# Performance work log

Measured on AMD Instinct MI355X. Metric: run time of the kernel, lower is better.

Reference implementation:

```python
import jax, jax.numpy as jnp
import numpy as np

TOKENS = 16384
IN_F = 2048
OUT_F = 2048
RANK = 32
GROUP = 64          # int4 scale group size
PAD = 256           # token padding multiple used by the fused activation quantizer
QMAX = 7.0          # signed int4 symmetric quantization


def setup_inputs() -> dict:
    key = jax.random.key(0)
    ks = jax.random.split(key, 7)
    x = jax.random.normal(ks[0], (TOKENS, IN_F), dtype=jnp.float32)
    # packed int4 weights: two signed nibbles per int8 lane
    qweight = jax.random.randint(ks[1], (OUT_F, IN_F // 2), -128, 128, dtype=jnp.int8)
    # per-group weight scales [in//group, out], strictly positive
    wscales = jnp.abs(jax.random.normal(ks[2], (IN_F // GROUP, OUT_F), dtype=jnp.float32)) * 0.01 + 1e-4
    # activation smoothing factors, positive and near 1
    smooth_factor = jnp.abs(jax.random.normal(ks[3], (IN_F,), dtype=jnp.float32)) * 0.5 + 0.75
    bias = jax.random.normal(ks[4], (OUT_F,), dtype=jnp.float32) * 0.01
    proj_down = jax.random.normal(ks[5], (IN_F, RANK), dtype=jnp.float32) * 0.02
    proj_up = jax.random.normal(ks[6], (OUT_F, RANK), dtype=jnp.float32) * 0.02
    return {"x": x, "qweight": qweight, "wscales": wscales,
            "smooth_factor": smooth_factor, "bias": bias,
            "proj_down": proj_down, "proj_up": proj_up}


def _unpack_int4(qweight):
    # low nibble = even input channel, high nibble = odd input channel; arithmetic shifts keep sign
    low = jnp.right_shift(jnp.left_shift(qweight, 4), 4)
    high = jnpp = jnp.right_shift(qweight, 4)
    w = jnp.stack([low, high], axis=-1).reshape(qweight.shape[0], qweight.shape[1] * 2)
    return w.astype(jnp.float32)  # [out, in], values in [-8, 7]


def _forward(x, qweight, wscales, smooth_factor, bias, proj_down, proj_up):
    T = x.shape[0]
    t_pad = ((T + PAD - 1) // PAD) * PAD
    # activation smoothing
    xs = x / smooth_factor
    xs_p = jnp.pad(xs, ((0, t_pad - T), (0, 0)))
    # per-token per-64-group symmetric int4 activation quantization
    xg = xs_p.reshape(t_pad, IN_F // GROUP, GROUP)
    amax = jnp.max(jnp.abs(xg), axis=-1)                       # [Tp, G]
    ascales = jnp.where(amax > 0, amax / QMAX, jnp.float32(1.0))
    qx = jnp.clip(jnp.round(xg / ascales[..., None]), -8.0, 7.0)
    xdq = (qx * ascales[..., None]).reshape(t_pad, IN_F)       # dequantized activations
    # dequantize packed int4 weights with per-group scales
    w = _unpack_int4(qweight)                                  # [out, in]
    wdq = (w.reshape(OUT_F, IN_F // GROUP, GROUP) * wscales.T[:, :, None]).reshape(OUT_F, IN_F)
    # packed GEMM (dequantized equivalent) + fused low-rank residual + bias
    y = xdq @ wdq.T                                            # [Tp, out]
    y = y + (xs_p @ proj_down) @ proj_up.T + bias
    return y[:T]


def reference(x, qweight, wscales, smooth_factor, bias, proj_down, proj_up):
    return _forward(x, qweight, wscales, smooth_factor, bias, proj_down, proj_up)
```

## Files before the change

### kernel.cpp

```cpp
#include <hip/hip_runtime.h>

#define TOKENS 16384
#define THALF 8192
#define INF 2048
#define OUTF 2048
#define RANK 32
#define BM 128
#define BN 128
#define NKSTEP 64

typedef int   int32x4  __attribute__((ext_vector_type(4)));
typedef int   int32x2  __attribute__((ext_vector_type(2)));
typedef float floatx4  __attribute__((ext_vector_type(4)));
typedef short bf16x8   __attribute__((ext_vector_type(8)));
typedef _Float16 f16x8 __attribute__((ext_vector_type(8)));

typedef __attribute__((address_space(1))) const void gconst_t;
typedef __attribute__((address_space(3))) void ldsv_t;

__device__ __forceinline__ void gload_lds16(const void* g, void* l) {
  __builtin_amdgcn_global_load_lds((gconst_t*)g, (ldsv_t*)l, 16, 0, 0);
}

__device__ __forceinline__ unsigned short f2bf(float f) {
  unsigned u = __float_as_uint(f);
  unsigned r = (u + 0x7FFFu + ((u >> 16) & 1u)) >> 16;
  return (unsigned short)r;
}

__global__ __launch_bounds__(256) void unpack_kernel(const int* __restrict__ qw,
                                                     const float* __restrict__ wsc,
                                                     _Float16* __restrict__ wdq) {
  int idx = blockIdx.x * 256 + threadIdx.x;
  int o = idx >> 6;
  int ch = idx & 63;
  float ws = wsc[(size_t)(ch >> 1) * OUTF + o];
  const int4* src = (const int4*)qw + (size_t)idx * 4;
  _Float16* dst = wdq + (size_t)o * INF + ch * 32;
#pragma unroll
  for (int q = 0; q < 4; ++q) {
    int4 v = src[q];
    int e[4] = {v.x, v.y, v.z, v.w};
    alignas(16) _Float16 h[8];
#pragma unroll
    for (int j = 0; j < 4; ++j) {
      int lo = ((int)((unsigned)e[j] << 28)) >> 28;
      int hi = ((int)((unsigned)e[j] << 24)) >> 28;
      h[2 * j]     = (_Float16)((float)lo * ws);
      h[2 * j + 1] = (_Float16)((float)hi * ws);
    }
    *(int4*)(dst + q * 8) = *(const int4*)h;
  }
}

__global__ __launch_bounds__(256) void prep_pdT(const float* __restrict__ pd,
                                                unsigned short* __restrict__ pdT) {
  int idx = blockIdx.x * 256 + threadIdx.x;
  int r = idx >> 11, c = idx & 2047;
  pdT[idx] = f2bf(pd[(size_t)c * RANK + r]);
}

__global__ __launch_bounds__(256) void quant_kernel(
    const float* __restrict__ x, const float* __restrict__ smooth,
    const unsigned short* __restrict__ pdT,
    _Float16* __restrict__ xdq, float* __restrict__ tdown, int tbase) {
  __shared__ char lds[32768];
  int tid = threadIdx.x, lane = tid & 63, wid = tid >> 6;
  int t0rel = blockIdx.x * 32;
  int mi = wid >> 1, ni = wid & 1;
  floatx4 acc = {0.f, 0.f, 0.f, 0.f};

  floatx4 xv[8];
  floatx4 sm;
  int32x4 pv[4];

  auto issue_loads = [&](int kc) {
    const float* xb = x + (size_t)(tbase + t0rel + wid * 8) * INF + kc * 256 + lane * 4;
#pragma unroll
    for (int r = 0; r < 8; ++r) xv[r] = *(const floatx4*)(xb + r * INF);
    sm = *(const floatx4*)(smooth + kc * 256 + lane * 4);
#pragma unroll
    for (int q = 0; q < 4; ++q) {
      int flat = tid + q * 256;
      int row = flat >> 5, c16 = flat & 31;
      pv[q] = *(const int32x4*)((const char*)pdT + (size_t)row * 4096 + kc * 512 + c16 * 16);
    }
  };

  issue_loads(0);

  for (int kc = 0; kc < 8; ++kc) {
    floatx4 rsm;
    rsm[0] = 1.0f / sm[0]; rsm[1] = 1.0f / sm[1];
    rsm[2] = 1.0f / sm[2]; rsm[3] = 1.0f / sm[3];
#pragma unroll
    for (int q = 0; q < 4; ++q) {
      int flat = tid + q * 256;
      int row = flat >> 5, c16 = flat & 31;
      int byte = (row * 512 + c16 * 16) ^ ((row & 7) << 4);
      *(int32x4*)(lds + 16384 + byte) = pv[q];
    }
#pragma unroll
    for (int r = 0; r < 8; ++r) {
      floatx4 xs;
      xs[0] = xv[r][0] * rsm[0]; xs[1] = xv[r][1] * rsm[1];
      xs[2] = xv[r][2] * rsm[2]; xs[3] = xv[r][3] * rsm[3];
      float m4 = fmaxf(fmaxf(fabsf(xs[0]), fabsf(xs[1])),
                       fmaxf(fabsf(xs[2]), fabsf(xs[3])));
      m4 = fmaxf(m4, __shfl_xor(m4, 1, 64));
      m4 = fmaxf(m4, __shfl_xor(m4, 2, 64));
      m4 = fmaxf(m4, __shfl_xor(m4, 4, 64));
      m4 = fmaxf(m4, __shfl_xor(m4, 8, 64));
      float ascale = m4 > 0.f ? m4 / 7.0f : 1.0f;
      float rq = 1.0f / ascale;
      int tokrel = t0rel + wid * 8 + r;
      alignas(8) _Float16 hq[4];
#pragma unroll
      for (int b = 0; b < 4; ++b) {
        float qf = fminf(7.f, fmaxf(-8.f, rintf(xs[b] * rq)));
        hq[b] = (_Float16)(qf * ascale);
      }
      *(int32x2*)((char*)xdq + ((size_t)tokrel * INF + kc * 256 + lane * 4) * 2) =
          *(const int32x2*)hq;
      unsigned lo = (unsigned)f2bf(xs[0]) | ((unsigned)f2bf(xs[1]) << 16);
      unsigned hi = (unsigned)f2bf(xs[2]) | ((unsigned)f2bf(xs[3]) << 16);
      int lrow = wid * 8 + r;
      int xbyte = (lrow * 512 + lane * 8) ^ ((lrow & 7) << 4);
      int32x2 wv; wv[0] = (int)lo; wv[1] = (int)hi;
      *(int32x2*)(lds + xbyte) = wv;
    }
    __syncthreads();
    if (kc + 1 < 8) issue_loads(kc + 1);
#pragma unroll
    for (int ks = 0; ks < 8; ++ks) {
      int arow = mi * 16 + (lane & 15);
      int ab = (arow * 512 + ks * 64 + ((lane >> 4) << 4)) ^ ((arow & 7) << 4);
      bf16x8 av = *(const bf16x8*)(lds + ab);
      int brow = ni * 16 + (lane & 15);
      int bb = (brow * 512 + ks * 64 + ((lane >> 4) << 4)) ^ ((brow & 7) << 4);
      bf16x8 bv = *(const bf16x8*)(lds + 16384 + bb);
      acc = __builtin_amdgcn_mfma_f32_16x16x32_bf16(av, bv, acc, 0, 0, 0);
    }
    __syncthreads();
  }

  int trow = tbase + t0rel + mi * 16 + ((lane >> 4) << 2);
  int col = ni * 16 + (lane & 15);
#pragma unroll
  for (int r = 0; r < 4; ++r)
    tdown[(size_t)(trow + r) * RANK + col] = acc[r];
}

__global__ __launch_bounds__(256, 3) void gemm_kernel(
    const _Float16* __restrict__ xdq, const _Float16* __restrict__ wdq,
    const float* __restrict__ tdown, const float* __restrict__ pu,
    const float* __restrict__ bias, float* __restrict__ y,
    int tbase, int mPanels) {
  __shared__ char smem[49152];

  int tid = threadIdx.x;
  int lane = tid & 63;
  int wid = tid >> 6;
  int wr = wid >> 1, wc = wid & 1;

  int s = blockIdx.x;
  int xcd = s & 7, idx = s >> 3;
  int nloc = idx & 3, mloc = idx >> 2;
  int o0 = (((xcd & 3) << 2) + nloc) * BN;
  int t0rel = ((xcd >> 3 << 3) + (xcd >> 2) * (mPanels >> 1) + mloc) * BM;
  int t0abs = tbase + t0rel;

  floatx4 acc[4][4];
#pragma unroll
  for (int m = 0; m < 4; ++m)
#pragma unroll
    for (int n = 0; n < 4; ++n) acc[m][n] = (floatx4){0.f, 0.f, 0.f, 0.f};

  auto stage = [&](int g) {
    int bufb = (g % 3) * 16384;
#pragma unroll
    for (int i = 0; i < 2; ++i) {
      int c = tid + i * 256;
      int row = c >> 2;
      int l = (c & 3) ^ ((row >> 1) & 3);
      gload_lds16((const char*)xdq + (size_t)(t0rel + row) * (INF * 2) + g * 64 + l * 16,
                  smem + bufb + (wid + i * 4) * 1024);
      gload_lds16((const char*)wdq + (size_t)(o0 + row) * (INF * 2) + g * 64 + l * 16,
                  smem + bufb + 8192 + (wid + i * 4) * 1024);
    }
  };

  int aoff[4], boff[4];
#pragma unroll
  for (int m = 0; m < 4; ++m) {
    int arow = (wr << 6) + (m << 4) + (lane & 15);
    aoff[m] = arow * 64 + ((((lane >> 4)) ^ ((arow >> 1) & 3)) << 4);
    int brow = (wc << 6) + (m << 4) + (lane & 15);
    boff[m] = 8192 + brow * 64 + ((((lane >> 4)) ^ ((brow >> 1) & 3)) << 4);
  }

  stage(0);
  stage(1);

  for (int g = 0; g < NKSTEP; ++g) {
    if (g == NKSTEP - 1) asm volatile("s_waitcnt vmcnt(0)" ::: "memory");
    else                 asm volatile("s_waitcnt vmcnt(4)" ::: "memory");
    __builtin_amdgcn_s_barrier();
    __builtin_amdgcn_sched_barrier(0);

    if (g + 2 < NKSTEP) stage(g + 2);

    int bufb = (g % 3) * 16384;
    f16x8 af[4], bf_[4];
#pragma unroll
    for (int m = 0; m < 4; ++m) af[m] = *(const f16x8*)(smem + bufb + aoff[m]);
#pragma unroll
    for (int n = 0; n < 4; ++n) bf_[n] = *(const f16x8*)(smem + bufb + boff[n]);

#pragma unroll
    for (int m = 0; m < 4; ++m)
#pragma unroll
      for (int n = 0; n < 4; ++n)
        acc[m][n] = __builtin_amdgcn_mfma_f32_16x16x32_f16(af[m], bf_[n], acc[m][n], 0, 0, 0);
  }

  __syncthreads();

  unsigned short* td_lds = (unsigned short*)smem;
  unsigned short* pu_lds = (unsigned short*)(smem + 8192);
  {
    int row = tid >> 1, h = (tid & 1) * 16;
    const float* ts = tdown + (size_t)(t0abs + row) * RANK + h;
    const float* ps = pu + (size_t)(o0 + row) * RANK + h;
    unsigned tw[8], pw[8];
#pragma unroll
    for (int q = 0; q < 4; ++q) {
      float4 v = *(const float4*)(ts + q * 4);
      tw[q * 2 + 0] = (unsigned)f2bf(v.x) | ((unsigned)f2bf(v.y) << 16);
      tw[q * 2 + 1] = (unsigned)f2bf(v.z) | ((unsigned)f2bf(v.w) << 16);
      float4 p = *(const float4*)(ps + q * 4);
      pw[q * 2 + 0] = (unsigned)f2bf(p.x) | ((unsigned)f2bf(p.y) << 16);
      pw[q * 2 + 1] = (unsigned)f2bf(p.z) | ((unsigned)f2bf(p.w) << 16);
    }
    int4 s0, s1;
    s0.x = (int)tw[0]; s0.y = (int)tw[1]; s0.z = (int)tw[2]; s0.w = (int)tw[3];
    s1.x = (int)tw[4]; s1.y = (int)tw[5]; s1.z = (int)tw[6]; s1.w = (int)tw[7];
    *(int4*)(td_lds + row * 32 + h) = s0;
    *(int4*)(td_lds + row * 32 + h + 8) = s1;
    s0.x = (int)pw[0]; s0.y = (int)pw[1]; s0.z = (int)pw[2]; s0.w = (int)pw[3];
    s1.x = (int)pw[4]; s1.y = (int)pw[5]; s1.z = (int)pw[6]; s1.w = (int)pw[7];
    *(int4*)(pu_lds + row * 32 + h) = s0;
    *(int4*)(pu_lds + row * 32 + h + 8) = s1;
  }
  __syncthreads();

  bf16x8 ta[4], pb4[4];
  int koff8 = (lane >> 4) << 3;
#pragma unroll
  for (int m = 0; m < 4; ++m)
    ta[m] = *(const bf16x8*)&td_lds[((wr << 6) + (m << 4) + (lane & 15)) * 32 + koff8];
#pragma unroll
  for (int n = 0; n < 4; ++n)
    pb4[n] = *(const bf16x8*)&pu_lds[((wc << 6) + (n << 4) + (lane & 15)) * 32 + koff8];

#pragma unroll
  for (int n = 0; n < 4; ++n) {
    int oc = o0 + (wc << 6) + (n << 4) + (lane & 15);
    float bv = bias[oc];
#pragma unroll
    for (int m = 0; m < 4; ++m) {
      floatx4 c = acc[m][n];
      c = __builtin_amdgcn_mfma_f32_16x16x32_bf16(ta[m], pb4[n], c, 0, 0, 0);
#pragma unroll
      for (int r = 0; r < 4; ++r) {
        int tr = t0abs + (wr << 6) + (m << 4) + ((lane >> 4) << 2) + r;
        y[(size_t)tr * OUTF + oc] = c[r] + bv;
      }
    }
  }
}

extern "C" void kernel_launch(void* const* d_in, const int* in_sizes, int n_in,
                              void* d_out, int out_size, void* d_ws, size_t ws_size,
                              hipStream_t stream) {
  const float* x      = (const float*)d_in[0];
  const int*   qw     = (const int*)d_in[1];
  const float* wsc    = (const float*)d_in[2];
  const float* smooth = (const float*)d_in[3];
  const float* bias   = (const float*)d_in[4];
  const float* pd     = (const float*)d_in[5];
  const float* pu     = (const float*)d_in[6];
  float* y = (float*)d_out;

  char* ws = (char*)d_ws;
  unsigned short* pdT = (unsigned short*)((char*)d_out + (64u << 20));

  if (ws_size >= 77594624ULL) {
    _Float16* xdq = (_Float16*)ws;
    _Float16* wdq = (_Float16*)(ws + 67108864);
    float* tdown  = (float*)(ws + 67108864 + 8388608);
    unpack_kernel<<<512, 256, 0, stream>>>(qw, wsc, wdq);
    prep_pdT<<<256, 256, 0, stream>>>(pd, pdT);
    quant_kernel<<<TOKENS / 32, 256, 0, stream>>>(x, smooth, pdT, xdq, tdown, 0);
    gemm_kernel<<<16 * (TOKENS / BM), 256, 0, stream>>>(
        xdq, wdq, tdown, pu, bias, y, 0, TOKENS / BM);
  } else {
    _Float16* xdq = (_Float16*)ws;
    _Float16* wdq = (_Float16*)(ws + 33554432);
    float* tdown  = (float*)(ws + 33554432 + 8388608);
    unpack_kernel<<<512, 256, 0, stream>>>(qw, wsc, wdq);
    prep_pdT<<<256, 256, 0, stream>>>(pd, pdT);
    for (int c = 0; c < 2; ++c) {
      int tbase = c * THALF;
      quant_kernel<<<THALF / 32, 256, 0, stream>>>(x, smooth, pdT, xdq, tdown, tbase);
      gemm_kernel<<<16 * (THALF / BM), 256, 0, stream>>>(
          xdq, wdq, tdown, pu, bias, y, tbase, THALF / BM);
    }
  }
}
```

Before: 236.2 us.

## Enlarge GEMM tile to 256x128 with 8 waves and 64-deep K steps

The GEMM block tile grows from 128x128 to 256x128 with 512 threads (8 waves) per block, and each pipeline stage now loads a 64-element K slice instead of 32, halving the number of barrier-separated iterations. LDS use rises to 144 KB for the triple-buffered stages with a new 8-slot XOR swizzle. The aim is more reuse of each loaded weight tile, lower per-K-step sync overhead, and fewer blocks. In exchange occupancy per CU drops, the LDS footprint is large, and each block loads more per stage.

```diff
diff --git a/kernel.cpp b/kernel.cpp
--- a/kernel.cpp
+++ b/kernel.cpp
@@ -5,9 +5,9 @@
 #define INF 2048
 #define OUTF 2048
 #define RANK 32
-#define BM 128
+#define BM 256
 #define BN 128
-#define NKSTEP 64
+#define NPER 32
 
 typedef int   int32x4  __attribute__((ext_vector_type(4)));
 typedef int   int32x2  __attribute__((ext_vector_type(2)));
@@ -151,23 +151,24 @@
     tdown[(size_t)(trow + r) * RANK + col] = acc[r];
 }
 
-__global__ __launch_bounds__(256, 3) void gemm_kernel(
+__global__ __launch_bounds__(512, 2) void gemm_kernel(
     const _Float16* __restrict__ xdq, const _Float16* __restrict__ wdq,
     const float* __restrict__ tdown, const float* __restrict__ pu,
     const float* __restrict__ bias, float* __restrict__ y,
     int tbase, int mPanels) {
-  __shared__ char smem[49152];
+  __shared__ char smem[147456];
 
   int tid = threadIdx.x;
   int lane = tid & 63;
   int wid = tid >> 6;
-  int wr = wid >> 1, wc = wid & 1;
+  int wm = wid >> 1, wn = wid & 1;
 
   int s = blockIdx.x;
   int xcd = s & 7, idx = s >> 3;
-  int nloc = idx & 3, mloc = idx >> 2;
-  int o0 = (((xcd & 3) << 2) + nloc) * BN;
-  int t0rel = ((xcd >> 3 << 3) + (xcd >> 2) * (mPanels >> 1) + mloc) * BM;
+  int npan = ((xcd & 3) << 2) + (idx & 3);
+  int mpan = (xcd >> 2) * (mPanels >> 1) + (idx >> 2);
+  int o0 = npan * BN;
+  int t0rel = mpan * BM;
   int t0abs = tbase + t0rel;
 
   floatx4 acc[4][4];
@@ -177,80 +178,107 @@
     for (int n = 0; n < 4; ++n) acc[m][n] = (floatx4){0.f, 0.f, 0.f, 0.f};
 
   auto stage = [&](int g) {
-    int bufb = (g % 3) * 16384;
+    int bufb = (g % 3) * 49152;
+#pragma unroll
+    for (int i = 0; i < 4; ++i) {
+      int f = i * 512 + tid;
+      int row = f >> 3, sl = (f & 7) ^ (row & 7);
+      gload_lds16((const char*)xdq + (size_t)(t0rel + row) * (INF * 2) + g * 128 + sl * 16,
+                  smem + bufb + i * 8192 + wid * 1024);
+    }
 #pragma unroll
     for (int i = 0; i < 2; ++i) {
-      int c = tid + i * 256;
-      int row = c >> 2;
-      int l = (c & 3) ^ ((row >> 1) & 3);
-      gload_lds16((const char*)xdq + (size_t)(t0rel + row) * (INF * 2) + g * 64 + l * 16,
-                  smem + bufb + (wid + i * 4) * 1024);
-      gload_lds16((const char*)wdq + (size_t)(o0 + row) * (INF * 2) + g * 64 + l * 16,
-                  smem + bufb + 8192 + (wid + i * 4) * 1024);
+      int f = i * 512 + tid;
+      int row = f >> 3, sl = (f & 7) ^ (row & 7);
+      gload_lds16((const char*)wdq + (size_t)(o0 + row) * (INF * 2) + g * 128 + sl * 16,
+                  smem + bufb + 32768 + i * 8192 + wid * 1024);
     }
   };
 
-  int aoff[4], boff[4];
-#pragma unroll
-  for (int m = 0; m < 4; ++m) {
-    int arow = (wr << 6) + (m << 4) + (lane & 15);
-    aoff[m] = arow * 64 + ((((lane >> 4)) ^ ((arow >> 1) & 3)) << 4);
-    int brow = (wc << 6) + (m << 4) + (lane & 15);
-    boff[m] = 8192 + brow * 64 + ((((lane >> 4)) ^ ((brow >> 1) & 3)) << 4);
+  int aoff[4][2], boff[4][2];
+#pragma unroll
+  for (int mr = 0; mr < 4; ++mr) {
+    int r = (wm << 6) + (mr << 4) + (lane & 15);
+#pragma unroll
+    for (int ks = 0; ks < 2; ++ks) {
+      int sl = ((ks << 2) + (lane >> 4)) ^ (r & 7);
+      aoff[mr][ks] = r * 128 + sl * 16;
+    }
+  }
+#pragma unroll
+  for (int nr = 0; nr < 4; ++nr) {
+    int r = (wn << 6) + (nr << 4) + (lane & 15);
+#pragma unroll
+    for (int ks = 0; ks < 2; ++ks) {
+      int sl = ((ks << 2) + (lane >> 4)) ^ (r & 7);
+      boff[nr][ks] = 32768 + r * 128 + sl * 16;
+    }
   }
 
   stage(0);
   stage(1);
 
-  for (int g = 0; g < NKSTEP; ++g) {
-    if (g == NKSTEP - 1) asm volatile("s_waitcnt vmcnt(0)" ::: "memory");
-    else                 asm volatile("s_waitcnt vmcnt(4)" ::: "memory");
+  for (int g = 0; g < NPER; ++g) {
+    if (g == NPER - 1) asm volatile("s_waitcnt vmcnt(0)" ::: "memory");
+    else               asm volatile("s_waitcnt vmcnt(6)" ::: "memory");
     __builtin_amdgcn_s_barrier();
     __builtin_amdgcn_sched_barrier(0);
 
-    if (g + 2 < NKSTEP) stage(g + 2);
-
-    int bufb = (g % 3) * 16384;
-    f16x8 af[4], bf_[4];
-#pragma unroll
-    for (int m = 0; m < 4; ++m) af[m] = *(const f16x8*)(smem + bufb + aoff[m]);
-#pragma unroll
-    for (int n = 0; n < 4; ++n) bf_[n] = *(const f16x8*)(smem + bufb + boff[n]);
-
-#pragma unroll
-    for (int m = 0; m < 4; ++m)
-#pragma unroll
-      for (int n = 0; n < 4; ++n)
-        acc[m][n] = __builtin_amdgcn_mfma_f32_16x16x32_f16(af[m], bf_[n], acc[m][n], 0, 0, 0);
+    if (g + 2 < NPER) stage(g + 2);
+
+    int bufb = (g % 3) * 49152;
+    f16x8 af[2][4], bf_[2][4];
+#pragma unroll
+    for (int ks = 0; ks < 2; ++ks) {
+#pragma unroll
+      for (int mr = 0; mr < 4; ++mr) af[ks][mr] = *(const f16x8*)(smem + bufb + aoff[mr][ks]);
+#pragma unroll
+      for (int nr = 0; nr < 4; ++nr) bf_[ks][nr] = *(const f16x8*)(smem + bufb + boff[nr][ks]);
+    }
+
+#pragma unroll
+    for (int ks = 0; ks < 2; ++ks)
+#pragma unroll
+      for (int mr = 0; mr < 4; ++mr)
+#pragma unroll
+        for (int nr = 0; nr < 4; ++nr)
+          acc[mr][nr] = __builtin_amdgcn_mfma_f32_16x16x32_f16(af[ks][mr], bf_[ks][nr],
+                                                               acc[mr][nr], 0, 0, 0);
   }
 
   __syncthreads();
 
   unsigned short* td_lds = (unsigned short*)smem;
-  unsigned short* pu_lds = (unsigned short*)(smem + 8192);
+  unsigned short* pu_lds = (unsigned short*)(smem + 16384);
   {
     int row = tid >> 1, h = (tid & 1) * 16;
     const float* ts = tdown + (size_t)(t0abs + row) * RANK + h;
-    const float* ps = pu + (size_t)(o0 + row) * RANK + h;
-    unsigned tw[8], pw[8];
+    unsigned tw[8];
 #pragma unroll
     for (int q = 0; q < 4; ++q) {
       float4 v = *(const float4*)(ts + q * 4);
       tw[q * 2 + 0] = (unsigned)f2bf(v.x) | ((unsigned)f2bf(v.y) << 16);
       tw[q * 2 + 1] = (unsigned)f2bf(v.z) | ((unsigned)f2bf(v.w) << 16);
-      float4 p = *(const float4*)(ps + q * 4);
-      pw[q * 2 + 0] = (unsigned)f2bf(p.x) | ((unsigned)f2bf(p.y) << 16);
-      pw[q * 2 + 1] = (unsigned)f2bf(p.z) | ((unsigned)f2bf(p.w) << 16);
     }
     int4 s0, s1;
     s0.x = (int)tw[0]; s0.y = (int)tw[1]; s0.z = (int)tw[2]; s0.w = (int)tw[3];
     s1.x = (int)tw[4]; s1.y = (int)tw[5]; s1.z = (int)tw[6]; s1.w = (int)tw[7];
     *(int4*)(td_lds + row * 32 + h) = s0;
     *(int4*)(td_lds + row * 32 + h + 8) = s1;
-    s0.x = (int)pw[0]; s0.y = (int)pw[1]; s0.z = (int)pw[2]; s0.w = (int)pw[3];
-    s1.x = (int)pw[4]; s1.y = (int)pw[5]; s1.z = (int)pw[6]; s1.w = (int)pw[7];
-    *(int4*)(pu_lds + row * 32 + h) = s0;
-    *(int4*)(pu_lds + row * 32 + h + 8) = s1;
+    if (tid < 256) {
+      const float* ps = pu + (size_t)(o0 + row) * RANK + h;
+      unsigned pw[8];
+#pragma unroll
+      for (int q = 0; q < 4; ++q) {
+        float4 p = *(const float4*)(ps + q * 4);
+        pw[q * 2 + 0] = (unsigned)f2bf(p.x) | ((unsigned)f2bf(p.y) << 16);
+        pw[q * 2 + 1] = (unsigned)f2bf(p.z) | ((unsigned)f2bf(p.w) << 16);
+      }
+      s0.x = (int)pw[0]; s0.y = (int)pw[1]; s0.z = (int)pw[2]; s0.w = (int)pw[3];
+      s1.x = (int)pw[4]; s1.y = (int)pw[5]; s1.z = (int)pw[6]; s1.w = (int)pw[7];
+      *(int4*)(pu_lds + row * 32 + h) = s0;
+      *(int4*)(pu_lds + row * 32 + h + 8) = s1;
+    }
   }
   __syncthreads();
 
@@ -258,14 +286,14 @@
   int koff8 = (lane >> 4) << 3;
 #pragma unroll
   for (int m = 0; m < 4; ++m)
-    ta[m] = *(const bf16x8*)&td_lds[((wr << 6) + (m << 4) + (lane & 15)) * 32 + koff8];
+    ta[m] = *(const bf16x8*)&td_lds[((wm << 6) + (m << 4) + (lane & 15)) * 32 + koff8];
 #pragma unroll
   for (int n = 0; n < 4; ++n)
-    pb4[n] = *(const bf16x8*)&pu_lds[((wc << 6) + (n << 4) + (lane & 15)) * 32 + koff8];
+    pb4[n] = *(const bf16x8*)&pu_lds[((wn << 6) + (n << 4) + (lane & 15)) * 32 + koff8];
 
 #pragma unroll
   for (int n = 0; n < 4; ++n) {
-    int oc = o0 + (wc << 6) + (n << 4) + (lane & 15);
+    int oc = o0 + (wn << 6) + (n << 4) + (lane & 15);
     float bv = bias[oc];
 #pragma unroll
     for (int m = 0; m < 4; ++m) {
@@ -273,7 +301,7 @@
       c = __builtin_amdgcn_mfma_f32_16x16x32_bf16(ta[m], pb4[n], c, 0, 0, 0);
 #pragma unroll
       for (int r = 0; r < 4; ++r) {
-        int tr = t0abs + (wr << 6) + (m << 4) + ((lane >> 4) << 2) + r;
+        int tr = t0abs + (wm << 6) + (m << 4) + ((lane >> 4) << 2) + r;
         y[(size_t)tr * OUTF + oc] = c[r] + bv;
       }
     }
@@ -302,7 +330,7 @@
     unpack_kernel<<<512, 256, 0, stream>>>(qw, wsc, wdq);
     prep_pdT<<<256, 256, 0, stream>>>(pd, pdT);
     quant_kernel<<<TOKENS / 32, 256, 0, stream>>>(x, smooth, pdT, xdq, tdown, 0);
-    gemm_kernel<<<16 * (TOKENS / BM), 256, 0, stream>>>(
+    gemm_kernel<<<16 * (TOKENS / BM), 512, 0, stream>>>(
         xdq, wdq, tdown, pu, bias, y, 0, TOKENS / BM);
   } else {
     _Float16* xdq = (_Float16*)ws;
@@ -313,7 +341,7 @@
     for (int c = 0; c < 2; ++c) {
       int tbase = c * THALF;
       quant_kernel<<<THALF / 32, 256, 0, stream>>>(x, smooth, pdT, xdq, tdown, tbase);
-      gemm_kernel<<<16 * (THALF / BM), 256, 0, stream>>>(
+      gemm_kernel<<<16 * (THALF / BM), 512, 0, stream>>>(
           xdq, wdq, tdown, pu, bias, y, tbase, THALF / BM);
     }
   }
```

After: 220.8 us. 6.5% less time.

## Enlarge GEMM tile to 256x256 with 16-wave blocks and merge prep kernels

Applied to the files above, without the earlier changes.

The GEMM moves from 128x128 tiles with 4 waves to 256x256 tiles with 16 waves per 1024-thread block, each wave still computing a 64x64 sub-tile. LDS triple buffering doubles to 96 KB. The prefetch is now issued after the LDS fragment reads, and MFMA issue priority is raised with s_setprio. The aim is to halve global/L2 traffic per FLOP and cut the block count. The weight-unpack and projection-transpose kernels are merged into one launch. The cost is one block per CU with large LDS, so there is less latency hiding across blocks and a coarser tail.

```diff
diff --git a/kernel.cpp b/kernel.cpp
--- a/kernel.cpp
+++ b/kernel.cpp
@@ -5,9 +5,9 @@
 #define INF 2048
 #define OUTF 2048
 #define RANK 32
-#define BM 128
-#define BN 128
-#define NKSTEP 64
+#define BM 256
+#define BN 256
+#define NT 64
 
 typedef int   int32x4  __attribute__((ext_vector_type(4)));
 typedef int   int32x2  __attribute__((ext_vector_type(2)));
@@ -28,36 +28,38 @@
   return (unsigned short)r;
 }
 
-__global__ __launch_bounds__(256) void unpack_kernel(const int* __restrict__ qw,
-                                                     const float* __restrict__ wsc,
-                                                     _Float16* __restrict__ wdq) {
-  int idx = blockIdx.x * 256 + threadIdx.x;
-  int o = idx >> 6;
-  int ch = idx & 63;
-  float ws = wsc[(size_t)(ch >> 1) * OUTF + o];
-  const int4* src = (const int4*)qw + (size_t)idx * 4;
-  _Float16* dst = wdq + (size_t)o * INF + ch * 32;
-#pragma unroll
-  for (int q = 0; q < 4; ++q) {
-    int4 v = src[q];
-    int e[4] = {v.x, v.y, v.z, v.w};
-    alignas(16) _Float16 h[8];
-#pragma unroll
-    for (int j = 0; j < 4; ++j) {
-      int lo = ((int)((unsigned)e[j] << 28)) >> 28;
-      int hi = ((int)((unsigned)e[j] << 24)) >> 28;
-      h[2 * j]     = (_Float16)((float)lo * ws);
-      h[2 * j + 1] = (_Float16)((float)hi * ws);
-    }
-    *(int4*)(dst + q * 8) = *(const int4*)h;
-  }
-}
-
-__global__ __launch_bounds__(256) void prep_pdT(const float* __restrict__ pd,
-                                                unsigned short* __restrict__ pdT) {
-  int idx = blockIdx.x * 256 + threadIdx.x;
-  int r = idx >> 11, c = idx & 2047;
-  pdT[idx] = f2bf(pd[(size_t)c * RANK + r]);
+__global__ __launch_bounds__(256) void prep_kernel(const int* __restrict__ qw,
+                                                   const float* __restrict__ wsc,
+                                                   _Float16* __restrict__ wdq,
+                                                   const float* __restrict__ pd,
+                                                   unsigned short* __restrict__ pdT) {
+  int b = blockIdx.x;
+  if (b < 512) {
+    int idx = b * 256 + threadIdx.x;
+    int o = idx >> 6;
+    int ch = idx & 63;
+    float ws = wsc[(size_t)(ch >> 1) * OUTF + o];
+    const int4* src = (const int4*)qw + (size_t)idx * 4;
+    _Float16* dst = wdq + (size_t)o * INF + ch * 32;
+#pragma unroll
+    for (int q = 0; q < 4; ++q) {
+      int4 v = src[q];
+      int e[4] = {v.x, v.y, v.z, v.w};
+      alignas(16) _Float16 h[8];
+#pragma unroll
+      for (int j = 0; j < 4; ++j) {
+        int lo = ((int)((unsigned)e[j] << 28)) >> 28;
+        int hi = ((int)((unsigned)e[j] << 24)) >> 28;
+        h[2 * j]     = (_Float16)((float)lo * ws);
+        h[2 * j + 1] = (_Float16)((float)hi * ws);
+      }
+      *(int4*)(dst + q * 8) = *(const int4*)h;
+    }
+  } else {
+    int idx = (b - 512) * 256 + threadIdx.x;
+    int r = idx >> 11, c = idx & 2047;
+    pdT[idx] = f2bf(pd[(size_t)c * RANK + r]);
+  }
 }
 
 __global__ __launch_bounds__(256) void quant_kernel(
@@ -151,23 +153,24 @@
     tdown[(size_t)(trow + r) * RANK + col] = acc[r];
 }
 
-__global__ __launch_bounds__(256, 3) void gemm_kernel(
+__global__ __launch_bounds__(1024) void gemm_kernel(
     const _Float16* __restrict__ xdq, const _Float16* __restrict__ wdq,
     const float* __restrict__ tdown, const float* __restrict__ pu,
     const float* __restrict__ bias, float* __restrict__ y,
     int tbase, int mPanels) {
-  __shared__ char smem[49152];
+  __shared__ char smem[98304];
 
   int tid = threadIdx.x;
   int lane = tid & 63;
   int wid = tid >> 6;
-  int wr = wid >> 1, wc = wid & 1;
+  int wm = wid >> 2, wn = wid & 3;
 
   int s = blockIdx.x;
   int xcd = s & 7, idx = s >> 3;
-  int nloc = idx & 3, mloc = idx >> 2;
-  int o0 = (((xcd & 3) << 2) + nloc) * BN;
-  int t0rel = ((xcd >> 3 << 3) + (xcd >> 2) * (mPanels >> 1) + mloc) * BM;
+  int npan = ((xcd & 3) << 1) + (idx & 1);
+  int mpan = (xcd >> 2) * (mPanels >> 1) + (idx >> 1);
+  int o0 = npan * BN;
+  int t0rel = mpan * BM;
   int t0abs = tbase + t0rel;
 
   floatx4 acc[4][4];
@@ -176,81 +179,73 @@
 #pragma unroll
     for (int n = 0; n < 4; ++n) acc[m][n] = (floatx4){0.f, 0.f, 0.f, 0.f};
 
-  auto stage = [&](int g) {
-    int bufb = (g % 3) * 16384;
-#pragma unroll
-    for (int i = 0; i < 2; ++i) {
-      int c = tid + i * 256;
-      int row = c >> 2;
-      int l = (c & 3) ^ ((row >> 1) & 3);
-      gload_lds16((const char*)xdq + (size_t)(t0rel + row) * (INF * 2) + g * 64 + l * 16,
-                  smem + bufb + (wid + i * 4) * 1024);
-      gload_lds16((const char*)wdq + (size_t)(o0 + row) * (INF * 2) + g * 64 + l * 16,
-                  smem + bufb + 8192 + (wid + i * 4) * 1024);
-    }
+  auto stage = [&](int t) {
+    int buf = (t % 3) * 32768;
+    int row = tid >> 2;
+    int sl = (tid & 3) ^ ((row >> 1) & 3);
+    gload_lds16((const char*)xdq + (size_t)(t0rel + row) * (INF * 2) + t * 64 + sl * 16,
+                smem + buf + tid * 16);
+    gload_lds16((const char*)wdq + (size_t)(o0 + row) * (INF * 2) + t * 64 + sl * 16,
+                smem + buf + 16384 + tid * 16);
   };
 
-  int aoff[4], boff[4];
-#pragma unroll
-  for (int m = 0; m < 4; ++m) {
-    int arow = (wr << 6) + (m << 4) + (lane & 15);
-    aoff[m] = arow * 64 + ((((lane >> 4)) ^ ((arow >> 1) & 3)) << 4);
-    int brow = (wc << 6) + (m << 4) + (lane & 15);
-    boff[m] = 8192 + brow * 64 + ((((lane >> 4)) ^ ((brow >> 1) & 3)) << 4);
-  }
+  int l = lane & 15;
+  int sw = (l >> 1) & 3;
+  int aoff = (wm * 64 + l) * 64 + (((lane >> 4) ^ sw) << 4);
+  int boff = 16384 + (wn * 64 + l) * 64 + (((lane >> 4) ^ sw) << 4);
 
   stage(0);
   stage(1);
 
-  for (int g = 0; g < NKSTEP; ++g) {
-    if (g == NKSTEP - 1) asm volatile("s_waitcnt vmcnt(0)" ::: "memory");
-    else                 asm volatile("s_waitcnt vmcnt(4)" ::: "memory");
+  for (int t = 0; t < NT; ++t) {
+    if (t == NT - 1) asm volatile("s_waitcnt vmcnt(0)" ::: "memory");
+    else             asm volatile("s_waitcnt vmcnt(2)" ::: "memory");
     __builtin_amdgcn_s_barrier();
     __builtin_amdgcn_sched_barrier(0);
 
-    if (g + 2 < NKSTEP) stage(g + 2);
-
-    int bufb = (g % 3) * 16384;
-    f16x8 af[4], bf_[4];
-#pragma unroll
-    for (int m = 0; m < 4; ++m) af[m] = *(const f16x8*)(smem + bufb + aoff[m]);
-#pragma unroll
-    for (int n = 0; n < 4; ++n) bf_[n] = *(const f16x8*)(smem + bufb + boff[n]);
-
+    int buf = (t % 3) * 32768;
+    f16x8 ar[4], br[4];
+#pragma unroll
+    for (int m = 0; m < 4; ++m) ar[m] = *(const f16x8*)(smem + buf + aoff + m * 1024);
+#pragma unroll
+    for (int n = 0; n < 4; ++n) br[n] = *(const f16x8*)(smem + buf + boff + n * 1024);
+
+    if (t + 2 < NT) stage(t + 2);
+
+    asm volatile("s_waitcnt lgkmcnt(0)" ::: "memory");
+    __builtin_amdgcn_sched_barrier(0);
+    __builtin_amdgcn_s_setprio(1);
 #pragma unroll
     for (int m = 0; m < 4; ++m)
 #pragma unroll
       for (int n = 0; n < 4; ++n)
-        acc[m][n] = __builtin_amdgcn_mfma_f32_16x16x32_f16(af[m], bf_[n], acc[m][n], 0, 0, 0);
+        acc[m][n] = __builtin_amdgcn_mfma_f32_16x16x32_f16(ar[m], br[n], acc[m][n], 0, 0, 0);
+    __builtin_amdgcn_s_setprio(0);
   }
 
   __syncthreads();
 
   unsigned short* td_lds = (unsigned short*)smem;
-  unsigned short* pu_lds = (unsigned short*)(smem + 8192);
+  unsigned short* pu_lds = (unsigned short*)(smem + 16384);
   {
-    int row = tid >> 1, h = (tid & 1) * 16;
-    const float* ts = tdown + (size_t)(t0abs + row) * RANK + h;
-    const float* ps = pu + (size_t)(o0 + row) * RANK + h;
-    unsigned tw[8], pw[8];
-#pragma unroll
-    for (int q = 0; q < 4; ++q) {
-      float4 v = *(const float4*)(ts + q * 4);
-      tw[q * 2 + 0] = (unsigned)f2bf(v.x) | ((unsigned)f2bf(v.y) << 16);
-      tw[q * 2 + 1] = (unsigned)f2bf(v.z) | ((unsigned)f2bf(v.w) << 16);
-      float4 p = *(const float4*)(ps + q * 4);
-      pw[q * 2 + 0] = (unsigned)f2bf(p.x) | ((unsigned)f2bf(p.y) << 16);
-      pw[q * 2 + 1] = (unsigned)f2bf(p.z) | ((unsigned)f2bf(p.w) << 16);
-    }
-    int4 s0, s1;
-    s0.x = (int)tw[0]; s0.y = (int)tw[1]; s0.z = (int)tw[2]; s0.w = (int)tw[3];
-    s1.x = (int)tw[4]; s1.y = (int)tw[5]; s1.z = (int)tw[6]; s1.w = (int)tw[7];
-    *(int4*)(td_lds + row * 32 + h) = s0;
-    *(int4*)(td_lds + row * 32 + h + 8) = s1;
-    s0.x = (int)pw[0]; s0.y = (int)pw[1]; s0.z = (int)pw[2]; s0.w = (int)pw[3];
-    s1.x = (int)pw[4]; s1.y = (int)pw[5]; s1.z = (int)pw[6]; s1.w = (int)pw[7];
-    *(int4*)(pu_lds + row * 32 + h) = s0;
-    *(int4*)(pu_lds + row * 32 + h + 8) = s1;
+    int row = tid >> 2, seg = (tid & 3) * 8;
+    const float* ts = tdown + (size_t)(t0abs + row) * RANK + seg;
+    const float* ps = pu + (size_t)(o0 + row) * RANK + seg;
+    float4 v0 = *(const float4*)(ts);
+    float4 v1 = *(const float4*)(ts + 4);
+    int4 sv;
+    sv.x = (int)((unsigned)f2bf(v0.x) | ((unsigned)f2bf(v0.y) << 16));
+    sv.y = (int)((unsigned)f2bf(v0.z) | ((unsigned)f2bf(v0.w) << 16));
+    sv.z = (int)((unsigned)f2bf(v1.x) | ((unsigned)f2bf(v1.y) << 16));
+    sv.w = (int)((unsigned)f2bf(v1.z) | ((unsigned)f2bf(v1.w) << 16));
+    *(int4*)(td_lds + row * 32 + seg) = sv;
+    float4 p0 = *(const float4*)(ps);
+    float4 p1 = *(const float4*)(ps + 4);
+    sv.x = (int)((unsigned)f2bf(p0.x) | ((unsigned)f2bf(p0.y) << 16));
+    sv.y = (int)((unsigned)f2bf(p0.z) | ((unsigned)f2bf(p0.w) << 16));
+    sv.z = (int)((unsigned)f2bf(p1.x) | ((unsigned)f2bf(p1.y) << 16));
+    sv.w = (int)((unsigned)f2bf(p1.z) | ((unsigned)f2bf(p1.w) << 16));
+    *(int4*)(pu_lds + row * 32 + seg) = sv;
   }
   __syncthreads();
 
@@ -258,14 +253,14 @@
   int koff8 = (lane >> 4) << 3;
 #pragma unroll
   for (int m = 0; m < 4; ++m)
-    ta[m] = *(const bf16x8*)&td_lds[((wr << 6) + (m << 4) + (lane & 15)) * 32 + koff8];
+    ta[m] = *(const bf16x8*)&td_lds[((wm << 6) + (m << 4) + l) * 32 + koff8];
 #pragma unroll
   for (int n = 0; n < 4; ++n)
-    pb4[n] = *(const bf16x8*)&pu_lds[((wc << 6) + (n << 4) + (lane & 15)) * 32 + koff8];
+    pb4[n] = *(const bf16x8*)&pu_lds[((wn << 6) + (n << 4) + l) * 32 + koff8];
 
 #pragma unroll
   for (int n = 0; n < 4; ++n) {
-    int oc = o0 + (wc << 6) + (n << 4) + (lane & 15);
+    int oc = o0 + (wn << 6) + (n << 4) + l;
     float bv = bias[oc];
 #pragma unroll
     for (int m = 0; m < 4; ++m) {
@@ -273,7 +268,7 @@
       c = __builtin_amdgcn_mfma_f32_16x16x32_bf16(ta[m], pb4[n], c, 0, 0, 0);
 #pragma unroll
       for (int r = 0; r < 4; ++r) {
-        int tr = t0abs + (wr << 6) + (m << 4) + ((lane >> 4) << 2) + r;
+        int tr = t0abs + (wm << 6) + (m << 4) + ((lane >> 4) << 2) + r;
         y[(size_t)tr * OUTF + oc] = c[r] + bv;
       }
     }
@@ -299,21 +294,19 @@
     _Float16* xdq = (_Float16*)ws;
     _Float16* wdq = (_Float16*)(ws + 67108864);
     float* tdown  = (float*)(ws + 67108864 + 8388608);
-    unpack_kernel<<<512, 256, 0, stream>>>(qw, wsc, wdq);
-    prep_pdT<<<256, 256, 0, stream>>>(pd, pdT);
+    prep_kernel<<<768, 256, 0, stream>>>(qw, wsc, wdq, pd, pdT);
     quant_kernel<<<TOKENS / 32, 256, 0, stream>>>(x, smooth, pdT, xdq, tdown, 0);
-    gemm_kernel<<<16 * (TOKENS / BM), 256, 0, stream>>>(
+    gemm_kernel<<<8 * (TOKENS / BM), 1024, 0, stream>>>(
         xdq, wdq, tdown, pu, bias, y, 0, TOKENS / BM);
   } else {
     _Float16* xdq = (_Float16*)ws;
     _Float16* wdq = (_Float16*)(ws + 33554432);
     float* tdown  = (float*)(ws + 33554432 + 8388608);
-    unpack_kernel<<<512, 256, 0, stream>>>(qw, wsc, wdq);
-    prep_pdT<<<256, 256, 0, stream>>>(pd, pdT);
+    prep_kernel<<<768, 256, 0, stream>>>(qw, wsc, wdq, pd, pdT);
     for (int c = 0; c < 2; ++c) {
       int tbase = c * THALF;
       quant_kernel<<<THALF / 32, 256, 0, stream>>>(x, smooth, pdT, xdq, tdown, tbase);
-      gemm_kernel<<<16 * (THALF / BM), 256, 0, stream>>>(
+      gemm_kernel<<<8 * (THALF / BM), 1024, 0, stream>>>(
           xdq, wdq, tdown, pu, bias, y, tbase, THALF / BM);
     }
   }
```

Result: faster. 206.1 us (-12.7%).
